# Performance work log

Hardware: AMD Instinct MI355X
Metric: run time of the kernel (lower is better)

## Reference

```python
import jax, jax.numpy as jnp
import numpy as np


def _gelu(x):
    # tf.nn.gelu default is exact (non-approximate)
    return jax.nn.gelu(x, approximate=False)


def _conv1d_same(x, w, b, stride):
    # x: [B, T, Cin], w: [K, Cin, Cout] -> [B, T', Cout], TF 'SAME' padding
    y = jax.lax.conv_general_dilated(
        x, w, window_strides=(stride,), padding='SAME',
        dimension_numbers=('NWC', 'WIO', 'NWC'))
    return y + b


def _pos_encoding(seq_len, d_model, dtype):
    pos = jnp.arange(seq_len, dtype=jnp.float32)[:, None]
    i = jnp.arange(d_model)[None, :]
    angle = pos / jnp.power(10000.0, (2 * (i // 2)).astype(jnp.float32) / d_model)
    pe = jnp.where(i % 2 == 0, jnp.sin(angle), jnp.cos(angle))
    return pe.astype(dtype)  # [seq_len, d_model]


def _lstm(x, Wk, Wr, b):
    # x: [B, S, F]; Keras gate order i, f, g(c), o. Inference: dropout is no-op.
    B = x.shape[0]
    H = Wr.shape[0]

    def step(carry, xt):
        h, c = carry
        z = xt @ Wk + h @ Wr + b  # [B, 4H]
        i, f, g, o = jnp.split(z, 4, axis=-1)
        c = jax.nn.sigmoid(f) * c + jax.nn.sigmoid(i) * jnp.tanh(g)
        h = jax.nn.sigmoid(o) * jnp.tanh(c)
        return (h, c), h

    h0 = jnp.zeros((B, H), x.dtype)
    (_, _), hs = jax.lax.scan(step, (h0, h0), jnp.swapaxes(x, 0, 1))
    return jnp.swapaxes(hs, 0, 1)  # [B, S, H]


def setup_inputs() -> dict:
    key = jax.random.key(0)
    ks = jax.random.split(key, 8)
    B, T, Cin = 8, 2000, 128
    D = 512
    x = jax.random.normal(ks[0], (B, T, Cin), dtype=jnp.float32)
    conv1_w = jax.random.normal(ks[1], (3, Cin, 4096), dtype=jnp.float32) * 0.02
    conv1_b = jnp.zeros((4096,), dtype=jnp.float32)
    conv2_w = jax.random.normal(ks[2], (3, 4096, 1024), dtype=jnp.float32) * 0.02
    conv2_b = jnp.zeros((1024,), dtype=jnp.float32)
    Fin = T // 2  # LSTM feature dim after stride-2 conv + permute
    lstm_k = jax.random.normal(ks[3], (Fin, 4 * D), dtype=jnp.float32) * 0.02
    lstm_r = jax.random.normal(ks[4], (D, 4 * D), dtype=jnp.float32) * 0.02
    lstm_b = jnp.zeros((4 * D,), dtype=jnp.float32).at[D:2 * D].set(1.0)  # unit_forget_bias
    return dict(x=x, conv1_w=conv1_w, conv1_b=conv1_b, conv2_w=conv2_w,
                conv2_b=conv2_b, lstm_k=lstm_k, lstm_r=lstm_r, lstm_b=lstm_b)


def reference(x, conv1_w, conv1_b, conv2_w, conv2_b, lstm_k, lstm_r, lstm_b):
    h = _gelu(_conv1d_same(x, conv1_w, conv1_b, 1))      # [B, T, 4096]
    h = _gelu(_conv1d_same(h, conv2_w, conv2_b, 2))      # [B, T/2, 1024]
    h = jnp.transpose(h, (0, 2, 1))                      # [B, 1024, T/2]
    out = _lstm(h, lstm_k, lstm_r, lstm_b)               # [B, 1024, D]
    pe = _pos_encoding(out.shape[1], out.shape[2], out.dtype)
    return out + pe[None, :, :]
```

## Files before the change

### kernel.cpp

```cpp
#include <hip/hip_runtime.h>
#include <cmath>
#include <cstdint>

typedef __bf16 bf16;
typedef __bf16 bf16x8 __attribute__((ext_vector_type(8)));
typedef float f32x4 __attribute__((ext_vector_type(4)));

static __device__ __forceinline__ float gelu_exact(float x) {
    return 0.5f * x * (1.f + erff(x * 0.70710678118654752f));
}

static __device__ __forceinline__ float fast_sigmoid(float x) {
    return __builtin_amdgcn_rcpf(1.f + __expf(-x));
}
static __device__ __forceinline__ float fast_tanh(float x) {
    return 1.f - 2.f * __builtin_amdgcn_rcpf(1.f + __expf(2.f * x));
}

static __device__ __forceinline__ void store16_sc1(float* p, f32x4 v) {
    asm volatile("global_store_dwordx4 %0, %1, off sc1" :: "v"(p), "v"(v) : "memory");
}
static __device__ __forceinline__ void load64_sc1(const float* p, f32x4& a, f32x4& b,
                                                  f32x4& c, f32x4& d) {
    asm volatile(
        "global_load_dwordx4 %0, %4, off sc1\n\t"
        "global_load_dwordx4 %1, %4, off offset:16 sc1\n\t"
        "global_load_dwordx4 %2, %4, off offset:32 sc1\n\t"
        "global_load_dwordx4 %3, %4, off offset:48 sc1\n\t"
        "s_waitcnt vmcnt(0)"
        : "=&v"(a), "=&v"(b), "=&v"(c), "=&v"(d)
        : "v"(p) : "memory");
}

__global__ void cvt_xpad_kernel(const float* __restrict__ x, bf16* __restrict__ xp) {
    int idx = blockIdx.x * 256 + threadIdx.x;
    if (idx >= 8 * 2002 * 128) return;
    int c = idx & 127;
    int rest = idx >> 7;
    int tp = rest % 2002;
    int b = rest / 2002;
    float v = 0.f;
    if (tp >= 1 && tp <= 2000) v = x[(b * 2000 + tp - 1) * 128 + c];
    xp[idx] = (bf16)v;
}

template <typename OT>
__global__ void transpose_cvt_kernel(const float* __restrict__ in, OT* __restrict__ out,
                                     int R, int C, int Rpad) {
    __shared__ float tile[32][33];
    int tx = threadIdx.x & 31, ty = threadIdx.x >> 5;
    int r0 = blockIdx.y * 32, c0 = blockIdx.x * 32;
    for (int i = ty; i < 32; i += 8) {
        int r = r0 + i, c = c0 + tx;
        tile[i][tx] = (r < R && c < C) ? in[(size_t)r * C + c] : 0.f;
    }
    __syncthreads();
    for (int i = ty; i < 32; i += 8) {
        int c = c0 + i, r = r0 + tx;
        if (c < C && r < Rpad) out[(size_t)c * Rpad + r] = (OT)tile[tx][i];
    }
}

__global__ void transpose_split_kernel(const float* __restrict__ in, bf16* __restrict__ hi,
                                       bf16* __restrict__ lo, int R, int C) {
    __shared__ float tile[32][33];
    int tx = threadIdx.x & 31, ty = threadIdx.x >> 5;
    int r0 = blockIdx.y * 32, c0 = blockIdx.x * 32;
    for (int i = ty; i < 32; i += 8) {
        int r = r0 + i, c = c0 + tx;
        tile[i][tx] = (r < R && c < C) ? in[(size_t)r * C + c] : 0.f;
    }
    __syncthreads();
    for (int i = ty; i < 32; i += 8) {
        int c = c0 + i, r = r0 + tx;
        if (c < C && r < R) {
            float v = tile[tx][i];
            bf16 h = (bf16)v;
            size_t o = (size_t)c * R + r;
            hi[o] = h;
            lo[o] = (bf16)(v - (float)h);
        }
    }
}

__global__ void zero_aux_kernel(bf16* __restrict__ h1, unsigned int* __restrict__ flagsP) {
    int idx = blockIdx.x * 256 + threadIdx.x;
    if (idx < 8 * 4096) {
        int b = idx >> 12, n = idx & 4095;
        h1[((size_t)(b * 2001 + 2000)) * 4096 + n] = (bf16)0.f;
    }
    int m = idx - 8 * 4096;
    if (m >= 0 && m < 64 * 32) flagsP[m] = 0u;
}

template <int MODE>
__launch_bounds__(256)
__global__ void gemm_kernel(const bf16* __restrict__ A, const bf16* __restrict__ BT,
                            const float* __restrict__ bias, void* __restrict__ Cout) {
    constexpr int KTOT = (MODE == 0) ? 384 : (MODE == 1) ? 12288 : 1024;
    constexpr int MTOT = (MODE == 0) ? 16000 : (MODE == 1) ? 8000 : 8192;
    __shared__ __align__(16) bf16 As[128 * 32];
    __shared__ __align__(16) bf16 Bs[128 * 32];
    const int tid = threadIdx.x;
    const int lane = tid & 63, wave = tid >> 6;
    const int m0 = blockIdx.y * 128, n0 = blockIdx.x * 128;
    const int wm = (wave >> 1) * 64, wn = (wave & 1) * 64;

    f32x4 acc[4][4];
#pragma unroll
    for (int mi = 0; mi < 4; ++mi)
#pragma unroll
        for (int ni = 0; ni < 4; ++ni) acc[mi][ni] = (f32x4){0.f, 0.f, 0.f, 0.f};

    for (int kt = 0; kt < KTOT / 32; ++kt) {
        const int k0 = kt * 32;
        __syncthreads();
#pragma unroll
        for (int s = 0; s < 2; ++s) {
            int ch = tid + s * 256;
            int row = ch >> 2;
            int ko = (ch & 3) * 8;
            int m = m0 + row;
            if (m > MTOT - 1) m = MTOT - 1;
            const bf16* ga;
            if (MODE == 0) {
                int b = m / 2000, t = m - b * 2000;
                ga = A + ((size_t)(b * 2002 + t + (k0 >> 7)) * 128 + (k0 & 127) + ko);
            } else if (MODE == 1) {
                int b = m / 1000, t = m - b * 1000;
                ga = A + ((size_t)(b * 2001 + 2 * t + (k0 >> 12)) * 4096 + (k0 & 4095) + ko);
            } else {
                ga = A + ((size_t)m * 1000 + k0 + ko);
            }
            *(uint4*)&As[ch * 8] = *(const uint4*)ga;
            const bf16* gb = BT + ((size_t)(n0 + row) * KTOT + k0 + ko);
            *(uint4*)&Bs[ch * 8] = *(const uint4*)gb;
        }
        __syncthreads();
        bf16x8 af[4], bfr[4];
#pragma unroll
        for (int i = 0; i < 4; ++i)
            af[i] = *(const bf16x8*)&As[(wm + i * 16 + (lane & 15)) * 32 + (lane >> 4) * 8];
#pragma unroll
        for (int i = 0; i < 4; ++i)
            bfr[i] = *(const bf16x8*)&Bs[(wn + i * 16 + (lane & 15)) * 32 + (lane >> 4) * 8];
#pragma unroll
        for (int mi = 0; mi < 4; ++mi)
#pragma unroll
            for (int ni = 0; ni < 4; ++ni)
                acc[mi][ni] = __builtin_amdgcn_mfma_f32_16x16x32_bf16(af[mi], bfr[ni], acc[mi][ni], 0, 0, 0);
    }

#pragma unroll
    for (int mi = 0; mi < 4; ++mi) {
        int rb = m0 + wm + mi * 16 + (lane >> 4) * 4;
#pragma unroll
        for (int ni = 0; ni < 4; ++ni) {
            int col = n0 + wn + ni * 16 + (lane & 15);
#pragma unroll
            for (int i = 0; i < 4; ++i) {
                int row = rb + i;
                float v = acc[mi][ni][i];
                if (MODE == 0) {
                    float y = gelu_exact(v + bias[col]);
                    int b = row / 2000, t = row - b * 2000;
                    ((bf16*)Cout)[(size_t)(b * 2001 + t) * 4096 + col] = (bf16)y;
                } else if (MODE == 1) {
                    if (row < 8000) {
                        float y = gelu_exact(v + bias[col]);
                        int b = row / 1000, t = row - b * 1000;
                        ((bf16*)Cout)[(size_t)(b * 1024 + col) * 1000 + t] = (bf16)y;
                    }
                } else {
                    ((float*)Cout)[(size_t)row * 2048 + col] = v + bias[col];
                }
            }
        }
    }
}

__launch_bounds__(256, 1)
__global__ void lstm_persist_kernel(const float* __restrict__ Zin,
                                    const bf16* __restrict__ WrHi,
                                    const bf16* __restrict__ WrLo,
                                    float* __restrict__ hstep,
                                    unsigned int* __restrict__ flagsP,
                                    float* __restrict__ out) {
    __shared__ __align__(16) unsigned char hS[2][8192];
    __shared__ float zex[4][128];
    const int tid = threadIdx.x;
    const int wv = tid >> 6;
    const int w = blockIdx.x;
    const int lane = tid & 63;

    bf16x8 bh[16], bl[16];
    {
        const size_t cb = (size_t)(wv * 512 + w * 16 + (lane & 15)) * 512 + (lane >> 4) * 8;
#pragma unroll
        for (int kk = 0; kk < 16; ++kk) {
            bh[kk] = *(const bf16x8*)&WrHi[cb + kk * 32];
            bl[kk] = *(const bf16x8*)&WrLo[cb + kk * 32];
        }
    }

    const int b = tid >> 4, u = tid & 15, j = w * 16 + u;
    float c_state = 0.f;
    float zin0 = 0.f, zin1 = 0.f, zin2 = 0.f, zin3 = 0.f;
    const float invf = powf(10000.f, -(float)(2 * (j >> 1)) * (1.f / 512.f));
    if (tid < 128) {
        const float* zp = Zin + (size_t)(b * 1024) * 2048;
        zin0 = zp[j]; zin1 = zp[512 + j]; zin2 = zp[1024 + j]; zin3 = zp[1536 + j];
    }

    const int rowsel = lane & 15;
    const int kq = lane >> 4;
    const unsigned aswz = (unsigned)((rowsel & 7) << 4);
    const unsigned abase = (unsigned)((rowsel & 7) * 1024);

    const int srow = tid >> 5;
    const int scol = tid & 31;
    const unsigned ssw = (unsigned)((srow & 7) << 4);
    const unsigned sbase = (unsigned)(srow * 1024);

    for (int t = 0; t < 1024; ++t) {
        if (t > 0) {
            if (wv == 3) {
                const unsigned tgt = (unsigned)t;
                for (;;) {
                    unsigned f = __hip_atomic_load(&flagsP[lane * 32], __ATOMIC_RELAXED,
                                                   __HIP_MEMORY_SCOPE_AGENT);
                    if (__all((int)(f >= tgt))) break;
                    __builtin_amdgcn_s_sleep(1);
                }
            }
            __syncthreads();
        }
        {
            float v[16];
            if (t > 0) {
                f32x4 va, vb, vc, vd;
                load64_sc1(hstep + (size_t)t * 4096 + srow * 512 + scol * 16, va, vb, vc, vd);
#pragma unroll
                for (int i = 0; i < 4; ++i) {
                    v[i] = va[i]; v[4 + i] = vb[i]; v[8 + i] = vc[i]; v[12 + i] = vd[i];
                }
            } else {
#pragma unroll
                for (int i = 0; i < 16; ++i) v[i] = 0.f;
            }
            bf16x8 hi0, hi1, lo0, lo1;
#pragma unroll
            for (int i = 0; i < 8; ++i) {
                bf16 h0 = (bf16)v[i];
                hi0[i] = h0; lo0[i] = (bf16)(v[i] - (float)h0);
                bf16 h1 = (bf16)v[8 + i];
                hi1[i] = h1; lo1[i] = (bf16)(v[8 + i] - (float)h1);
            }
            unsigned o0 = (unsigned)(scol * 32);
            *(bf16x8*)&hS[0][sbase + (o0 ^ ssw)] = hi0;
            *(bf16x8*)&hS[0][sbase + ((o0 + 16) ^ ssw)] = hi1;
            *(bf16x8*)&hS[1][sbase + (o0 ^ ssw)] = lo0;
            *(bf16x8*)&hS[1][sbase + ((o0 + 16) ^ ssw)] = lo1;
        }
        __syncthreads();
        f32x4 acc0 = {0.f, 0.f, 0.f, 0.f}, acc1 = {0.f, 0.f, 0.f, 0.f}, acc2 = {0.f, 0.f, 0.f, 0.f};
#pragma unroll
        for (int kk = 0; kk < 16; ++kk) {
            unsigned ko = (unsigned)((kk * 4 + kq) * 16);
            bf16x8 ah = *(const bf16x8*)&hS[0][abase + (ko ^ aswz)];
            bf16x8 al = *(const bf16x8*)&hS[1][abase + (ko ^ aswz)];
            acc0 = __builtin_amdgcn_mfma_f32_16x16x32_bf16(ah, bh[kk], acc0, 0, 0, 0);
            acc1 = __builtin_amdgcn_mfma_f32_16x16x32_bf16(al, bh[kk], acc1, 0, 0, 0);
            acc2 = __builtin_amdgcn_mfma_f32_16x16x32_bf16(ah, bl[kk], acc2, 0, 0, 0);
        }
        if (kq < 2) {
#pragma unroll
            for (int i = 0; i < 4; ++i)
                zex[wv][(kq * 4 + i) * 16 + rowsel] = acc0[i] + acc1[i] + acc2[i];
        }
        __syncthreads();
        if (tid < 128) {
            float zi = zex[0][tid] + zin0;
            float zf = zex[1][tid] + zin1;
            float zg = zex[2][tid] + zin2;
            float zo = zex[3][tid] + zin3;
            float ig = fast_sigmoid(zi);
            float fg = fast_sigmoid(zf);
            float og = fast_sigmoid(zo);
            float c = fg * c_state + ig * fast_tanh(zg);
            c_state = c;
            float hval = og * fast_tanh(c);
            if (t < 1023) {
                float h1s = __shfl_down(hval, 1);
                float h2s = __shfl_down(hval, 2);
                float h3s = __shfl_down(hval, 3);
                if ((tid & 3) == 0) {
                    f32x4 hv = {hval, h1s, h2s, h3s};
                    store16_sc1(hstep + (size_t)(t + 1) * 4096 + b * 512 + j, hv);
                }
                asm volatile("s_waitcnt vmcnt(0)" ::: "memory");
                if (lane == 0)
                    __hip_atomic_store(&flagsP[(w * 2 + wv) * 32], (unsigned)(t + 1),
                                       __ATOMIC_RELAXED, __HIP_MEMORY_SCOPE_AGENT);
            }
            float ang = (float)t * invf;
            float pe = (j & 1) ? cosf(ang) : sinf(ang);
            out[(size_t)(b * 1024 + t) * 512 + j] = hval + pe;
            if (t < 1023) {
                const float* zp = Zin + (size_t)(b * 1024 + t + 1) * 2048;
                zin0 = zp[j]; zin1 = zp[512 + j]; zin2 = zp[1024 + j]; zin3 = zp[1536 + j];
            }
        }
    }
}

extern "C" void kernel_launch(void* const* d_in, const int* in_sizes, int n_in,
                              void* d_out, int out_size, void* d_ws, size_t ws_size,
                              hipStream_t stream) {
    const float* x  = (const float*)d_in[0];
    const float* w1 = (const float*)d_in[1];
    const float* b1 = (const float*)d_in[2];
    const float* w2 = (const float*)d_in[3];
    const float* b2 = (const float*)d_in[4];
    const float* wk = (const float*)d_in[5];
    const float* wr = (const float*)d_in[6];
    const float* lb = (const float*)d_in[7];
    float* out = (float*)d_out;

    uint8_t* ws = (uint8_t*)d_ws;
    size_t off = 0;
    auto alloc = [&](size_t bytes) {
        void* p = ws + off;
        off += (bytes + 255) & ~(size_t)255;
        return p;
    };
    bf16* xpad = (bf16*)alloc((size_t)8 * 2002 * 128 * 2);
    bf16* W1T  = (bf16*)alloc((size_t)4096 * 384 * 2);
    bf16* W2T  = (bf16*)alloc((size_t)1024 * 12288 * 2);
    bf16* WkT  = (bf16*)alloc((size_t)2048 * 1024 * 2);
    bf16* WrHi = (bf16*)alloc((size_t)2048 * 512 * 2);
    bf16* WrLo = (bf16*)alloc((size_t)2048 * 512 * 2);
    bf16* h1   = (bf16*)alloc((size_t)8 * 2001 * 4096 * 2);
    bf16* h2T  = (bf16*)alloc((size_t)8 * 1024 * 1000 * 2 + 256);
    float* Zin = (float*)alloc((size_t)8 * 1024 * 2048 * 4);
    unsigned int* flagsP = (unsigned int*)alloc((size_t)64 * 32 * 4);
    float* hstep = (float*)h1;

    cvt_xpad_kernel<<<(8 * 2002 * 128 + 255) / 256, 256, 0, stream>>>(x, xpad);
    transpose_cvt_kernel<bf16><<<dim3(128, 12), 256, 0, stream>>>(w1, W1T, 384, 4096, 384);
    transpose_cvt_kernel<bf16><<<dim3(32, 384), 256, 0, stream>>>(w2, W2T, 12288, 1024, 12288);
    transpose_cvt_kernel<bf16><<<dim3(64, 32), 256, 0, stream>>>(wk, WkT, 1000, 2048, 1024);
    transpose_split_kernel<<<dim3(64, 16), 256, 0, stream>>>(wr, WrHi, WrLo, 512, 2048);
    zero_aux_kernel<<<(8 * 4096 + 64 * 32 + 255) / 256, 256, 0, stream>>>(h1, flagsP);

    gemm_kernel<0><<<dim3(32, 125), 256, 0, stream>>>(xpad, W1T, b1, (void*)h1);
    gemm_kernel<1><<<dim3(8, 63), 256, 0, stream>>>(h1, W2T, b2, (void*)h2T);
    gemm_kernel<2><<<dim3(16, 64), 256, 0, stream>>>(h2T, WkT, lb, (void*)Zin);

    lstm_persist_kernel<<<32, 256, 0, stream>>>(Zin, WrHi, WrLo, hstep, flagsP, out);
}
```

Measured before the change: 3.759 ms.

## Replace LSTM step flags with poisoned-slot polling on packed hi/lo hidden state

The persistent LSTM kernel no longer uses per-wave flag counters plus a store-wait-then-flag handshake. Each step's hidden-state buffer is pre-filled with a poison pattern, and consumers poll the data itself until no poison word remains. Producers now store a packed bf16 hi/lo pair per element, so consumers unpack with shifts instead of recomputing the split. This removes one global round trip and the flag ordering per step on the serial critical path. It relies on 16-byte stores becoming visible whole and on real values never matching the poison bits, and it adds a poison fill pass.

New measurement: 3.257 ms. -13.4%, faster.

```diff
diff --git a/kernel.cpp b/kernel.cpp
--- a/kernel.cpp
+++ b/kernel.cpp
@@ -4,7 +4,11 @@
 
 typedef __bf16 bf16;
 typedef __bf16 bf16x8 __attribute__((ext_vector_type(8)));
+typedef unsigned short u16x8 __attribute__((ext_vector_type(8)));
 typedef float f32x4 __attribute__((ext_vector_type(4)));
+typedef unsigned u32x4 __attribute__((ext_vector_type(4)));
+
+#define HPOISON 0x7FC07FC0u
 
 static __device__ __forceinline__ float gelu_exact(float x) {
     return 0.5f * x * (1.f + erff(x * 0.70710678118654752f));
@@ -17,11 +21,11 @@
     return 1.f - 2.f * __builtin_amdgcn_rcpf(1.f + __expf(2.f * x));
 }
 
-static __device__ __forceinline__ void store16_sc1(float* p, f32x4 v) {
+static __device__ __forceinline__ void store16u_sc1(unsigned* p, u32x4 v) {
     asm volatile("global_store_dwordx4 %0, %1, off sc1" :: "v"(p), "v"(v) : "memory");
 }
-static __device__ __forceinline__ void load64_sc1(const float* p, f32x4& a, f32x4& b,
-                                                  f32x4& c, f32x4& d) {
+static __device__ __forceinline__ void load64u_sc1(const unsigned* p, u32x4& a, u32x4& b,
+                                                   u32x4& c, u32x4& d) {
     asm volatile(
         "global_load_dwordx4 %0, %4, off sc1\n\t"
         "global_load_dwordx4 %1, %4, off offset:16 sc1\n\t"
@@ -83,14 +87,20 @@
     }
 }
 
-__global__ void zero_aux_kernel(bf16* __restrict__ h1, unsigned int* __restrict__ flagsP) {
+__global__ void zero_aux_kernel(bf16* __restrict__ h1) {
     int idx = blockIdx.x * 256 + threadIdx.x;
     if (idx < 8 * 4096) {
         int b = idx >> 12, n = idx & 4095;
         h1[((size_t)(b * 2001 + 2000)) * 4096 + n] = (bf16)0.f;
     }
-    int m = idx - 8 * 4096;
-    if (m >= 0 && m < 64 * 32) flagsP[m] = 0u;
+}
+
+__global__ void poison_kernel(unsigned* __restrict__ hstep) {
+    size_t i = (size_t)blockIdx.x * 256 + threadIdx.x;
+    if (i < (size_t)1024 * 4096 / 4) {
+        u32x4 pz = {HPOISON, HPOISON, HPOISON, HPOISON};
+        *(u32x4*)(hstep + i * 4) = pz;
+    }
 }
 
 template <int MODE>
@@ -183,8 +193,7 @@
 __global__ void lstm_persist_kernel(const float* __restrict__ Zin,
                                     const bf16* __restrict__ WrHi,
                                     const bf16* __restrict__ WrLo,
-                                    float* __restrict__ hstep,
-                                    unsigned int* __restrict__ flagsP,
+                                    unsigned* __restrict__ hstep,
                                     float* __restrict__ out) {
     __shared__ __align__(16) unsigned char hS[2][8192];
     __shared__ float zex[4][128];
@@ -223,44 +232,40 @@
     const unsigned sbase = (unsigned)(srow * 1024);
 
     for (int t = 0; t < 1024; ++t) {
-        if (t > 0) {
-            if (wv == 3) {
-                const unsigned tgt = (unsigned)t;
+        {
+            unsigned vv[16];
+            if (t > 0) {
+                const unsigned* src = hstep + (size_t)t * 4096 + srow * 512 + scol * 16;
                 for (;;) {
-                    unsigned f = __hip_atomic_load(&flagsP[lane * 32], __ATOMIC_RELAXED,
-                                                   __HIP_MEMORY_SCOPE_AGENT);
-                    if (__all((int)(f >= tgt))) break;
+                    u32x4 qa, qb, qc, qd;
+                    load64u_sc1(src, qa, qb, qc, qd);
+#pragma unroll
+                    for (int i = 0; i < 4; ++i) {
+                        vv[i] = qa[i]; vv[4 + i] = qb[i]; vv[8 + i] = qc[i]; vv[12 + i] = qd[i];
+                    }
+                    bool ok = true;
+#pragma unroll
+                    for (int i = 0; i < 16; ++i) ok = ok && (vv[i] != HPOISON);
+                    if (ok) break;
                     __builtin_amdgcn_s_sleep(1);
                 }
-            }
-            __syncthreads();
-        }
-        {
-            float v[16];
-            if (t > 0) {
-                f32x4 va, vb, vc, vd;
-                load64_sc1(hstep + (size_t)t * 4096 + srow * 512 + scol * 16, va, vb, vc, vd);
-#pragma unroll
-                for (int i = 0; i < 4; ++i) {
-                    v[i] = va[i]; v[4 + i] = vb[i]; v[8 + i] = vc[i]; v[12 + i] = vd[i];
-                }
             } else {
 #pragma unroll
-                for (int i = 0; i < 16; ++i) v[i] = 0.f;
-            }
-            bf16x8 hi0, hi1, lo0, lo1;
+                for (int i = 0; i < 16; ++i) vv[i] = 0u;
+            }
+            u16x8 h0, h1v, l0, l1v;
 #pragma unroll
             for (int i = 0; i < 8; ++i) {
-                bf16 h0 = (bf16)v[i];
-                hi0[i] = h0; lo0[i] = (bf16)(v[i] - (float)h0);
-                bf16 h1 = (bf16)v[8 + i];
-                hi1[i] = h1; lo1[i] = (bf16)(v[8 + i] - (float)h1);
+                h0[i]  = (unsigned short)(vv[i] >> 16);
+                l0[i]  = (unsigned short)(vv[i] & 0xFFFFu);
+                h1v[i] = (unsigned short)(vv[8 + i] >> 16);
+                l1v[i] = (unsigned short)(vv[8 + i] & 0xFFFFu);
             }
             unsigned o0 = (unsigned)(scol * 32);
-            *(bf16x8*)&hS[0][sbase + (o0 ^ ssw)] = hi0;
-            *(bf16x8*)&hS[0][sbase + ((o0 + 16) ^ ssw)] = hi1;
-            *(bf16x8*)&hS[1][sbase + (o0 ^ ssw)] = lo0;
-            *(bf16x8*)&hS[1][sbase + ((o0 + 16) ^ ssw)] = lo1;
+            *(u16x8*)&hS[0][sbase + (o0 ^ ssw)] = h0;
+            *(u16x8*)&hS[0][sbase + ((o0 + 16) ^ ssw)] = h1v;
+            *(u16x8*)&hS[1][sbase + (o0 ^ ssw)] = l0;
+            *(u16x8*)&hS[1][sbase + ((o0 + 16) ^ ssw)] = l1v;
         }
         __syncthreads();
         f32x4 acc0 = {0.f, 0.f, 0.f, 0.f}, acc1 = {0.f, 0.f, 0.f, 0.f}, acc2 = {0.f, 0.f, 0.f, 0.f};
@@ -291,17 +296,17 @@
             c_state = c;
             float hval = og * fast_tanh(c);
             if (t < 1023) {
-                float h1s = __shfl_down(hval, 1);
-                float h2s = __shfl_down(hval, 2);
-                float h3s = __shfl_down(hval, 3);
+                bf16 hh = (bf16)hval;
+                bf16 hlo = (bf16)(hval - (float)hh);
+                unsigned pk = ((unsigned)*(unsigned short*)&hh << 16) |
+                              (unsigned)*(unsigned short*)&hlo;
+                unsigned p1 = (unsigned)__shfl_down((int)pk, 1);
+                unsigned p2 = (unsigned)__shfl_down((int)pk, 2);
+                unsigned p3 = (unsigned)__shfl_down((int)pk, 3);
                 if ((tid & 3) == 0) {
-                    f32x4 hv = {hval, h1s, h2s, h3s};
-                    store16_sc1(hstep + (size_t)(t + 1) * 4096 + b * 512 + j, hv);
+                    u32x4 hv = {pk, p1, p2, p3};
+                    store16u_sc1(hstep + (size_t)(t + 1) * 4096 + b * 512 + j, hv);
                 }
-                asm volatile("s_waitcnt vmcnt(0)" ::: "memory");
-                if (lane == 0)
-                    __hip_atomic_store(&flagsP[(w * 2 + wv) * 32], (unsigned)(t + 1),
-                                       __ATOMIC_RELAXED, __HIP_MEMORY_SCOPE_AGENT);
             }
             float ang = (float)t * invf;
             float pe = (j & 1) ? cosf(ang) : sinf(ang);
@@ -343,19 +348,19 @@
     bf16* h1   = (bf16*)alloc((size_t)8 * 2001 * 4096 * 2);
     bf16* h2T  = (bf16*)alloc((size_t)8 * 1024 * 1000 * 2 + 256);
     float* Zin = (float*)alloc((size_t)8 * 1024 * 2048 * 4);
-    unsigned int* flagsP = (unsigned int*)alloc((size_t)64 * 32 * 4);
-    float* hstep = (float*)h1;
+    unsigned* hstep = (unsigned*)h1;
 
     cvt_xpad_kernel<<<(8 * 2002 * 128 + 255) / 256, 256, 0, stream>>>(x, xpad);
     transpose_cvt_kernel<bf16><<<dim3(128, 12), 256, 0, stream>>>(w1, W1T, 384, 4096, 384);
     transpose_cvt_kernel<bf16><<<dim3(32, 384), 256, 0, stream>>>(w2, W2T, 12288, 1024, 12288);
     transpose_cvt_kernel<bf16><<<dim3(64, 32), 256, 0, stream>>>(wk, WkT, 1000, 2048, 1024);
     transpose_split_kernel<<<dim3(64, 16), 256, 0, stream>>>(wr, WrHi, WrLo, 512, 2048);
-    zero_aux_kernel<<<(8 * 4096 + 64 * 32 + 255) / 256, 256, 0, stream>>>(h1, flagsP);
+    zero_aux_kernel<<<(8 * 4096 + 255) / 256, 256, 0, stream>>>(h1);
 
     gemm_kernel<0><<<dim3(32, 125), 256, 0, stream>>>(xpad, W1T, b1, (void*)h1);
     gemm_kernel<1><<<dim3(8, 63), 256, 0, stream>>>(h1, W2T, b2, (void*)h2T);
+    poison_kernel<<<4096, 256, 0, stream>>>(hstep);
     gemm_kernel<2><<<dim3(16, 64), 256, 0, stream>>>(h2T, WkT, lb, (void*)Zin);
 
-    lstm_persist_kernel<<<32, 256, 0, stream>>>(Zin, WrHi, WrLo, hstep, flagsP, out);
-}
+    lstm_persist_kernel<<<32, 256, 0, stream>>>(Zin, WrHi, WrLo, hstep, out);
+}
```
